# Kernel tuning notes

Hardware: AMD Instinct MI355X
Metric: run time of the kernel (lower is better)

Reference implementation:

```python
import jax, jax.numpy as jnp
import numpy as np

B, S, E, H = 4, 2048, 1024, 16
D = E // H  # head dim = 64


def setup_inputs() -> dict:
    key = jax.random.key(0)
    ks = jax.random.split(key, 9)
    sc = 1.0 / np.sqrt(E)
    x = jax.random.normal(ks[0], (B, S, E), dtype=jnp.float32)
    # causal mask: 1 = keep, 0 = masked -> -inf (matches masked_fill(mask==0, -inf))
    mask = jnp.broadcast_to(jnp.tril(jnp.ones((S, S), dtype=jnp.int32)), (B, S, S))
    return {
        "x": x,
        "mask": mask,
        "wq": jax.random.normal(ks[1], (E, E), dtype=jnp.float32) * sc,
        "bq": jax.random.normal(ks[2], (E,), dtype=jnp.float32) * sc,
        "wk": jax.random.normal(ks[3], (E, E), dtype=jnp.float32) * sc,
        "bk": jax.random.normal(ks[4], (E,), dtype=jnp.float32) * sc,
        "wv": jax.random.normal(ks[5], (E, E), dtype=jnp.float32) * sc,
        "bv": jax.random.normal(ks[6], (E,), dtype=jnp.float32) * sc,
        "wo": jax.random.normal(ks[7], (E, E), dtype=jnp.float32) * sc,
        "bo": jax.random.normal(ks[8], (E,), dtype=jnp.float32) * sc,
    }


def reference(x, mask, wq, bq, wk, bk, wv, bv, wo, bo):
    # nn.Linear: y = x @ W^T + b
    def proj(w, b):
        y = jnp.einsum('bse,fe->bsf', x, w) + b
        return y.reshape(B, S, H, D).transpose(0, 2, 1, 3)  # [B,H,S,D]

    q = proj(wq, bq)
    k = proj(wk, bk)
    v = proj(wv, bv)
    denom = jnp.asarray(np.sqrt(D), dtype=x.dtype)
    score = jnp.einsum('bhqd,bhkd->bhqk', q, k) / denom  # [B,H,S,S]
    score = jnp.where(mask[:, None, :, :] == 0, jnp.asarray(-jnp.inf, score.dtype), score)
    attn = jax.nn.softmax(score, axis=-1)
    out = jnp.einsum('bhqk,bhkd->bhqd', attn, v)  # [B,H,S,D]
    out = out.transpose(0, 2, 1, 3).reshape(B, S, E)
    return jnp.einsum('bse,fe->bsf', out, wo) + bo
```

## Files before the change

### kernel.cpp

```cpp
#include <hip/hip_runtime.h>
#include <cstdint>
#include <cstddef>

typedef unsigned short u16;
typedef __bf16 bf16;
typedef bf16 bf16x8 __attribute__((ext_vector_type(8)));
typedef bf16 bf16x4 __attribute__((ext_vector_type(4)));
typedef float f32x4 __attribute__((ext_vector_type(4)));
typedef u16 u16x8 __attribute__((ext_vector_type(8)));
typedef u16 u16x4 __attribute__((ext_vector_type(4)));

#define ASYNC16(g, l) __builtin_amdgcn_global_load_lds( \
    (const __attribute__((address_space(1))) void*)(g), \
    (__attribute__((address_space(3))) void*)(l), 16, 0, 0)

#define FENCE asm volatile("" ::: "memory")
#define BARRIER do { FENCE; __builtin_amdgcn_s_barrier(); FENCE; } while (0)
#define WAITVM(n) asm volatile("s_waitcnt vmcnt(" #n ")" ::: "memory")

__device__ __forceinline__ u16 f2bf(float f) {
  bf16 h = (bf16)f;
  return __builtin_bit_cast(u16, h);
}

__device__ __forceinline__ u16x4 pk4(float a, float b, float c, float d) {
  bf16x4 v = { (bf16)a, (bf16)b, (bf16)c, (bf16)d };
  return __builtin_bit_cast(u16x4, v);
}

__device__ __forceinline__ void store_out(u16* p, float v) { *p = f2bf(v); }
__device__ __forceinline__ void store_out(float* p, float v) { *p = v; }

__device__ __forceinline__ f32x4 mfma16(bf16x8 a, bf16x8 b, f32x4 c) {
  return __builtin_amdgcn_mfma_f32_16x16x32_bf16(a, b, c, 0, 0, 0);
}

__global__ void prep(const float* __restrict__ x,  const float* __restrict__ wq,
                     const float* __restrict__ wk, const float* __restrict__ wv,
                     const float* __restrict__ wo, const float* __restrict__ bq,
                     const float* __restrict__ bk,
                     u16* __restrict__ xb, u16* __restrict__ wqkb,
                     u16* __restrict__ wvb, u16* __restrict__ wob,
                     float* __restrict__ bqk, float scl)
{
  const int bid = blockIdx.x, tid = threadIdx.x;
  if (bid < 8192) {
    int i = bid * 256 + tid;
    float4 v = ((const float4*)x)[i];
    ((u16x4*)xb)[i] = pk4(v.x, v.y, v.z, v.w);
  } else if (bid < 12288) {
    int wsel = (bid - 8192) >> 10;
    int i = ((bid - 8192) & 1023) * 256 + tid;
    const float* src = wsel == 0 ? wq : wsel == 1 ? wk : wsel == 2 ? wv : wo;
    u16* dst = wsel == 0 ? wqkb : wsel == 1 ? wqkb + 1048576 : wsel == 2 ? wvb : wob;
    float s = wsel == 0 ? scl : 1.0f;
    float4 v = ((const float4*)src)[i];
    ((u16x4*)dst)[i] = pk4(v.x * s, v.y * s, v.z * s, v.w * s);
  } else {
    for (int i = tid; i < 1024; i += 256) {
      bqk[i] = bq[i] * scl;
      bqk[1024 + i] = bk[i];
    }
  }
}

template <typename OutT>
__device__ __forceinline__ void gemm256(
    u16* sA, u16* sB,
    const u16* __restrict__ A, const u16* __restrict__ Bm,
    const float* __restrict__ bias_col, const float* __restrict__ bias_row,
    OutT* __restrict__ C, int M, int N, int K, int bm, int bn)
{
  const int tid = threadIdx.x;
  const int w = tid >> 6, lane = tid & 63;
  const int quad = lane >> 4, l15 = lane & 15;
  const int wr = w >> 2, wc = w & 3;

  const int srow = tid >> 3;
  const int sslot = (tid & 7) ^ (srow & 7);
  const u16* gA = A + (size_t)(bm * 256 + srow) * K + sslot * 8;
  const u16* gB = Bm + (size_t)(bn * 256 + srow) * K + sslot * 8;
  u16* dA = sA + tid * 8;
  u16* dB = sB + tid * 8;
  const size_t rK64 = (size_t)64 * K, rK128 = (size_t)128 * K;

  auto stageA = [&](int c, int h, int kt) {
    const u16* s = gA + h * rK128 + kt * 64;
    u16* d = dA + c * 16384 + h * 8192;
    ASYNC16(s, d);
    ASYNC16(s + rK64, d + 4096);
  };
  auto stageB = [&](int c, int h, int kt) {
    const u16* s = gB + h * rK128 + kt * 64;
    u16* d = dB + c * 16384 + h * 8192;
    ASYNC16(s, d);
    ASYNC16(s + rK64, d + 4096);
  };

  f32x4 acc[8][4] = {};
  bf16x8 af[4][2];
  bf16x8 bf0[2][2];
  bf16x8 bf1[2][2];

  const int aRow = (wr * 128 + l15) * 64;
  const int bRow = (wc * 64 + l15) * 64;
  const int sw0 = (quad ^ (l15 & 7)) * 8;

#define LDA8(SRC, MH) do { \
    _Pragma("unroll") \
    for (int i = 0; i < 4; i++) { \
      af[i][0] = *(const bf16x8*)((SRC) + aRow + ((MH)*4 + i) * 1024 + sw0); \
      af[i][1] = *(const bf16x8*)((SRC) + aRow + ((MH)*4 + i) * 1024 + (sw0 ^ 32)); \
    } } while (0)

#define LDB4(DST, SRC, NH) do { \
    _Pragma("unroll") \
    for (int j = 0; j < 2; j++) { \
      DST[j][0] = *(const bf16x8*)((SRC) + bRow + ((NH)*2 + j) * 1024 + sw0); \
      DST[j][1] = *(const bf16x8*)((SRC) + bRow + ((NH)*2 + j) * 1024 + (sw0 ^ 32)); \
    } } while (0)

#define MMQ8(MH, NH, BF) do { \
    __builtin_amdgcn_s_setprio(1); \
    _Pragma("unroll") \
    for (int i = 0; i < 4; i++) { \
      acc[(MH)*4+i][(NH)*2+0] = mfma16(af[i][0], BF[0][0], acc[(MH)*4+i][(NH)*2+0]); \
      acc[(MH)*4+i][(NH)*2+0] = mfma16(af[i][1], BF[0][1], acc[(MH)*4+i][(NH)*2+0]); \
      acc[(MH)*4+i][(NH)*2+1] = mfma16(af[i][0], BF[1][0], acc[(MH)*4+i][(NH)*2+1]); \
      acc[(MH)*4+i][(NH)*2+1] = mfma16(af[i][1], BF[1][1], acc[(MH)*4+i][(NH)*2+1]); \
    } \
    __builtin_amdgcn_s_setprio(0); \
  } while (0)

  const int NT = K >> 6, NI = NT >> 1;

  stageB(0, 0, 0); stageB(0, 1, 0);
  stageA(0, 0, 0); stageA(0, 1, 0);
  stageB(1, 0, 1); stageB(1, 1, 1);
  WAITVM(4);
  BARRIER;

  u16* sA0 = sA;         u16* sA1 = sA + 16384;
  u16* sB0 = sB;         u16* sB1 = sB + 16384;

  for (int t = 0; t < NI; ++t) {
    const int k1 = 2 * t + 1, kn = 2 * t + 2, kn1 = 2 * t + 3;
    const bool more = (t + 1 < NI);

    LDA8(sA0, 0); LDB4(bf0, sB0, 0);
    stageA(1, 0, k1);
    BARRIER;
    MMQ8(0, 0, bf0);
    BARRIER;

    LDB4(bf1, sB0, 1);
    stageA(1, 1, k1);
    BARRIER;
    MMQ8(0, 1, bf1);
    BARRIER;

    LDA8(sA0, 1);
    if (more) stageB(0, 0, kn);
    BARRIER;
    MMQ8(1, 1, bf1);
    BARRIER;

    if (more) { stageB(0, 1, kn); WAITVM(4); }
    else      { WAITVM(0); }
    BARRIER;
    MMQ8(1, 0, bf0);
    BARRIER;

    LDA8(sA1, 0); LDB4(bf0, sB1, 0);
    if (more) stageA(0, 0, kn);
    BARRIER;
    MMQ8(0, 0, bf0);
    BARRIER;

    LDB4(bf1, sB1, 1);
    if (more) stageA(0, 1, kn);
    BARRIER;
    MMQ8(0, 1, bf1);
    BARRIER;

    LDA8(sA1, 1);
    if (more) stageB(1, 0, kn1);
    BARRIER;
    MMQ8(1, 1, bf1);
    BARRIER;

    if (more) { stageB(1, 1, kn1); WAITVM(4); }
    BARRIER;
    MMQ8(1, 0, bf0);
    BARRIER;
  }

#pragma unroll
  for (int nt = 0; nt < 4; nt++) {
    const int cc = bn * 256 + wc * 64 + nt * 16 + l15;
    const float bc = bias_col ? bias_col[cc] : 0.f;
#pragma unroll
    for (int mt = 0; mt < 8; mt++) {
      const int r0 = bm * 256 + wr * 128 + mt * 16 + quad * 4;
      f32x4 v = acc[mt][nt];
#pragma unroll
      for (int ri = 0; ri < 4; ri++) {
        const float bb = bc + (bias_row ? bias_row[r0 + ri] : 0.f);
        store_out(&C[(size_t)(r0 + ri) * N + cc], v[ri] + bb);
      }
    }
  }
#undef LDA8
#undef LDB4
#undef MMQ8
}

template <typename OutT>
__device__ __forceinline__ void gemm128(
    u16* sA, u16* sB,
    const u16* __restrict__ A, const u16* __restrict__ Bm,
    const float* __restrict__ bias_col, const float* __restrict__ bias_row,
    OutT* __restrict__ C, int M, int N, int K, int bm, int bn)
{
  const int tid = threadIdx.x;
  const int w = tid >> 6, lane = tid & 63;
  const int quad = lane >> 4, l15 = lane & 15;
  const int wr = w >> 2, wc = w & 3;

  const int srow = tid >> 3;
  const int sslot = (tid & 7) ^ (srow & 7);
  const u16* gA = A + (size_t)(bm * 128 + srow) * K + sslot * 8;
  const u16* gB = Bm + (size_t)(bn * 256 + srow) * K + sslot * 8;
  u16* dA = sA + tid * 8;
  u16* dB = sB + tid * 8;
  const size_t rK64 = (size_t)64 * K;

  auto stage0 = [&](int c, int kt) {
    const u16* a = gA + kt * 64;
    u16* da = dA + c * 8192;
    ASYNC16(a, da);
    ASYNC16(a + rK64, da + 4096);
    ASYNC16(gB + kt * 64, dB + c * 16384);
  };
  auto stage1 = [&](int c, int kt) {
    const u16* b = gB + kt * 64;
    u16* db = dB + c * 16384;
    ASYNC16(b + rK64,     db + 4096);
    ASYNC16(b + 2 * rK64, db + 8192);
    ASYNC16(b + 3 * rK64, db + 12288);
  };

  f32x4 acc[4][4] = {};
  bf16x8 af[4][2];
  bf16x8 bfr[2][2];

  const int aRow = (wr * 64 + l15) * 64;
  const int bRow = (wc * 64 + l15) * 64;
  const int sw0 = (quad ^ (l15 & 7)) * 8;

#define LDA(SRC) do { \
    _Pragma("unroll") \
    for (int i = 0; i < 4; i++) { \
      af[i][0] = *(const bf16x8*)((SRC) + aRow + i * 1024 + sw0); \
      af[i][1] = *(const bf16x8*)((SRC) + aRow + i * 1024 + (sw0 ^ 32)); \
    } } while (0)

#define LDB(SRC, NH) do { \
    _Pragma("unroll") \
    for (int j = 0; j < 2; j++) { \
      bfr[j][0] = *(const bf16x8*)((SRC) + bRow + ((NH)*2 + j) * 1024 + sw0); \
      bfr[j][1] = *(const bf16x8*)((SRC) + bRow + ((NH)*2 + j) * 1024 + (sw0 ^ 32)); \
    } } while (0)

#define MMQ(NH) do { \
    __builtin_amdgcn_s_setprio(1); \
    _Pragma("unroll") \
    for (int i = 0; i < 4; i++) { \
      acc[i][(NH)*2+0] = mfma16(af[i][0], bfr[0][0], acc[i][(NH)*2+0]); \
      acc[i][(NH)*2+0] = mfma16(af[i][1], bfr[0][1], acc[i][(NH)*2+0]); \
      acc[i][(NH)*2+1] = mfma16(af[i][0], bfr[1][0], acc[i][(NH)*2+1]); \
      acc[i][(NH)*2+1] = mfma16(af[i][1], bfr[1][1], acc[i][(NH)*2+1]); \
    } \
    __builtin_amdgcn_s_setprio(0); \
  } while (0)

  const int NT = K >> 6;

  stage0(0, 0); stage1(0, 0);
  stage0(1, 1); stage1(1, 1);
  WAITVM(6);
  BARRIER;

  for (int t = 0; t < NT; ++t) {
    const int c = t % 3, c2 = (t + 2) % 3;
    const bool more = (t + 2 < NT);
    const u16* SA = sA + c * 8192;
    const u16* SB = sB + c * 16384;

    LDA(SA); LDB(SB, 0);
    if (more) stage0(c2, t + 2);
    BARRIER;
    MMQ(0);
    BARRIER;

    LDB(SB, 1);
    if (more) {
      stage1(c2, t + 2);
      WAITVM(6);
    } else if (t == NT - 2) {
      WAITVM(0);
    }
    BARRIER;
    MMQ(1);
    BARRIER;
  }

#pragma unroll
  for (int nh = 0; nh < 2; nh++) {
#pragma unroll
    for (int j = 0; j < 2; j++) {
      const int cc = bn * 256 + wc * 64 + nh * 32 + j * 16 + l15;
      const float bc = bias_col ? bias_col[cc] : 0.f;
#pragma unroll
      for (int i = 0; i < 4; i++) {
        const int r0 = bm * 128 + wr * 64 + i * 16 + quad * 4;
        f32x4 v = acc[i][nh * 2 + j];
#pragma unroll
        for (int ri = 0; ri < 4; ri++) {
          const float bb = bc + (bias_row ? bias_row[r0 + ri] : 0.f);
          store_out(&C[(size_t)(r0 + ri) * N + cc], v[ri] + bb);
        }
      }
    }
  }
#undef LDA
#undef LDB
#undef MMQ
}

__global__ __launch_bounds__(512, 2) void gemm_qkv(
    const u16* __restrict__ xb, const u16* __restrict__ wqkb,
    const u16* __restrict__ wvb, const float* __restrict__ bqk,
    const float* __restrict__ bv, u16* __restrict__ qk, u16* __restrict__ vt)
{
  __shared__ __align__(16) u16 pool[73728];
  const int id = blockIdx.x;
  if (id < 256) {
    gemm256<u16>(pool, pool + 32768, xb, wqkb, bqk, nullptr, qk,
                 8192, 2048, 1024, id >> 3, id & 7);
  } else {
    const int j = id - 256;
    gemm128<u16>(pool, pool + 24576, wvb, xb, nullptr, bv, vt,
                 1024, 8192, 1024, j & 7, j >> 3);
  }
}

__global__ __launch_bounds__(512, 2) void gemm_out(
    const u16* __restrict__ ctx, const u16* __restrict__ wob,
    const float* __restrict__ bo, float* __restrict__ out)
{
  __shared__ __align__(16) u16 sA[3 * 8192];
  __shared__ __align__(16) u16 sB[3 * 16384];
  const int id = blockIdx.x;
  gemm128<float>(sA, sB, ctx, wob, bo, nullptr, out, 8192, 1024, 1024,
                 id >> 2, id & 3);
}

__global__ __launch_bounds__(256, 2) void fattn(
    const u16* __restrict__ QK, const u16* __restrict__ VT, u16* __restrict__ ctx)
{
  __shared__ u16 Kt[2][128 * 64];
  __shared__ u16 Vt[2][64 * 128];
  __shared__ u16 Pt[4 * 32 * 32];

  const int tid = threadIdx.x;
  const int w = tid >> 6, lane = tid & 63;
  const int quad = lane >> 4, l15 = lane & 15;
  const int p = blockIdx.x, h = blockIdx.y, b = blockIdx.z;
  const int nA = p + 1;
  const int sBs = 15 - p;

  const u16* QKb = QK + (size_t)b * 2048 * 2048;
  const u16* Kg = QKb + 1024 + h * 64 + ((tid & 7) ^ ((tid >> 3) & 7)) * 8;
  const u16* Vg = VT + (size_t)(h * 64) * 8192 + b * 2048 +
                  ((tid & 15) ^ ((tid >> 4) & 15)) * 8;

  u16* Pw = Pt + w * 1024;

  bf16x8 ones;
#pragma unroll
  for (int j = 0; j < 8; j++) ones[j] = (bf16)1.0f;

  bf16x8 qfA[2][2], qfB[2][2], qcur[2][2];
#pragma unroll
  for (int mt = 0; mt < 2; mt++)
#pragma unroll
    for (int ks = 0; ks < 2; ks++) {
      qfA[mt][ks] = *(const bf16x8*)(QKb +
          (size_t)(p  * 128 + w * 32 + mt * 16 + l15) * 2048 +
          h * 64 + ks * 32 + quad * 8);
      qfB[mt][ks] = *(const bf16x8*)(QKb +
          (size_t)(sBs * 128 + w * 32 + mt * 16 + l15) * 2048 +
          h * 64 + ks * 32 + quad * 8);
      qcur[mt][ks] = qfA[mt][ks];
    }

  auto stage = [&](int bi, int t) {
#pragma unroll
    for (int s = 0; s < 4; s++) {
      ASYNC16(Kg + (size_t)(t * 128 + s * 32 + (tid >> 3)) * 2048,
              Kt[bi] + (s * 256 + w * 64) * 8);
      ASYNC16(Vg + (size_t)(s * 16 + (tid >> 4)) * 8192 + t * 128,
              Vt[bi] + (s * 256 + w * 64) * 8);
    }
  };

  f32x4 oacc[4][2] = {};
  f32x4 lacc[2] = {};

  auto epi = [&](int sIdx) {
#pragma unroll
    for (int mt = 0; mt < 2; mt++) {
      float rl = 1.0f / lacc[mt][0];
      size_t row = (size_t)b * 2048 + sIdx * 128 + w * 32 + mt * 16 + l15;
#pragma unroll
      for (int dt = 0; dt < 4; dt++) {
        u16x4 o = pk4(oacc[dt][mt][0] * rl, oacc[dt][mt][1] * rl,
                      oacc[dt][mt][2] * rl, oacc[dt][mt][3] * rl);
        *(u16x4*)(ctx + row * 1024 + h * 64 + dt * 16 + quad * 4) = o;
      }
    }
  };

  int sCur = p, tcur = 0;
  stage(0, 0);

  for (int u = 0; u < 17; ++u) {
    const int cur = u & 1;
    if (u < 16) {
      const int tn = (u + 1 == nA) ? 0 : tcur + 1;
      stage(cur ^ 1, tn);
      WAITVM(8);
    } else {
      WAITVM(0);
    }
    BARRIER;

    const u16* Kc = Kt[cur];
    const u16* Vc = Vt[cur];

    f32x4 st[2][8] = {};
#pragma unroll
    for (int ks = 0; ks < 2; ks++) {
      bf16x8 kf[8];
#pragma unroll
      for (int nt = 0; nt < 8; nt++) {
        int row = nt * 16 + l15;
        kf[nt] = *(const bf16x8*)(Kc + (row * 8 + ((ks * 4 + quad) ^ (row & 7))) * 8);
      }
#pragma unroll
      for (int nt = 0; nt < 8; nt++) {
        st[0][nt] = mfma16(kf[nt], qcur[0][ks], st[0][nt]);
        st[1][nt] = mfma16(kf[nt], qcur[1][ks], st[1][nt]);
      }
    }

    if (tcur == sCur) {
#pragma unroll
      for (int mt = 0; mt < 2; mt++) {
        const int qg = w * 32 + mt * 16 + l15;
#pragma unroll
        for (int nt = 0; nt < 8; nt++)
#pragma unroll
          for (int r = 0; r < 4; r++)
            if (nt * 16 + quad * 4 + r > qg) st[mt][nt][r] = -3e38f;
      }
    }
#pragma unroll
    for (int mt = 0; mt < 2; mt++)
#pragma unroll
      for (int nt = 0; nt < 8; nt++)
#pragma unroll
        for (int r = 0; r < 4; r++)
          st[mt][nt][r] = exp2f(st[mt][nt][r]);

#pragma unroll
    for (int hf = 0; hf < 2; hf++) {
#pragma unroll
      for (int ks = 0; ks < 2; ks++) {
#pragma unroll
        for (int mt = 0; mt < 2; mt++) {
          const int row = mt * 16 + l15;
          const int swz = (row >> 1) & 3;
#pragma unroll
          for (int j = 0; j < 2; j++) {
            int nt = hf * 4 + ks * 2 + j;
            u16x4 pkv = pk4(st[mt][nt][0], st[mt][nt][1], st[mt][nt][2], st[mt][nt][3]);
            int c = (j * 2 + (quad >> 1)) ^ swz;
            *(u16x4*)(Pw + (row << 5) + (c << 3) + ((quad & 1) << 2)) = pkv;
          }
        }
        const int cq = quad ^ ((l15 >> 1) & 3);
        bf16x8 pf0 = *(const bf16x8*)(Pw + (l15 << 5) + (cq << 3));
        bf16x8 pf1 = *(const bf16x8*)(Pw + ((16 + l15) << 5) + (cq << 3));
        lacc[0] = mfma16(ones, pf0, lacc[0]);
        lacc[1] = mfma16(ones, pf1, lacc[1]);
#pragma unroll
        for (int dt = 0; dt < 4; dt++) {
          int vrow = dt * 16 + l15;
          bf16x8 vf = *(const bf16x8*)(Vc + (vrow * 16 + ((hf * 8 + ks * 4 + quad) ^ (vrow & 15))) * 8);
          oacc[dt][0] = mfma16(vf, pf0, oacc[dt][0]);
          oacc[dt][1] = mfma16(vf, pf1, oacc[dt][1]);
        }
      }
    }
    BARRIER;

    if (u == nA - 1) {
      epi(p);
#pragma unroll
      for (int dt = 0; dt < 4; dt++) {
        oacc[dt][0] = f32x4{0.f, 0.f, 0.f, 0.f};
        oacc[dt][1] = f32x4{0.f, 0.f, 0.f, 0.f};
      }
      lacc[0] = f32x4{0.f, 0.f, 0.f, 0.f};
      lacc[1] = f32x4{0.f, 0.f, 0.f, 0.f};
#pragma unroll
      for (int mt = 0; mt < 2; mt++)
#pragma unroll
        for (int ks = 0; ks < 2; ks++) qcur[mt][ks] = qfB[mt][ks];
      sCur = sBs; tcur = 0;
    } else {
      tcur++;
    }
  }

  epi(sBs);
}

extern "C" void kernel_launch(void* const* d_in, const int* in_sizes, int n_in,
                              void* d_out, int out_size, void* d_ws, size_t ws_size,
                              hipStream_t stream)
{
  const float* x  = (const float*)d_in[0];
  const float* wq = (const float*)d_in[2];
  const float* bq = (const float*)d_in[3];
  const float* wk = (const float*)d_in[4];
  const float* bk = (const float*)d_in[5];
  const float* wv = (const float*)d_in[6];
  const float* bv = (const float*)d_in[7];
  const float* wo = (const float*)d_in[8];
  const float* bo = (const float*)d_in[9];

  const float SCL = 0.125f * 1.44269504088896f;

  char* ws = (char*)d_ws;
  u16*   xb   = (u16*)(ws);
  u16*   ctx  = (u16*)(ws);
  u16*   wqkb = (u16*)(ws + 16777216);
  u16*   wvb  = (u16*)(ws + 20971520);
  u16*   wob  = (u16*)(ws + 23068672);
  float* bqk  = (float*)(ws + 25165824);
  u16*   qk   = (u16*)(ws + 25174016);
  u16*   vt   = (u16*)(ws + 58728448);
  float* out  = (float*)d_out;

  prep<<<12289, 256, 0, stream>>>(x, wq, wk, wv, wo, bq, bk,
                                  xb, wqkb, wvb, wob, bqk, SCL);

  gemm_qkv<<<512, 512, 0, stream>>>(xb, wqkb, wvb, bqk, bv, qk, vt);
  fattn<<<dim3(8, 16, 4), 256, 0, stream>>>(qk, vt, ctx);
  gemm_out<<<256, 512, 0, stream>>>(ctx, wob, bo, out);
}
```

Measured before the change: 313.4 us.

## Split attention blocks into 64-row query tiles with single-buffered K/V

The flash-attention kernel now runs 128-thread blocks (2 waves) that each handle a pair of 64-row query tiles (p and 31-p), so the causal work stays balanced across a grid twice as large. K/V staging drops from double-buffered to a single buffer, and the diagonal mask gains a row-parity offset. The launch grid is reordered so heads are the fastest-varying dimension. The intent is more resident blocks and less LDS per block, giving higher occupancy to hide latency. In exchange the loads are no longer overlapped with the MFMA work inside a block, and each K/V tile is now fetched once per 64 query rows instead of once per 128.

After: 306.9 us. 2.1% less time.

```diff
diff --git a/kernel.cpp b/kernel.cpp
--- a/kernel.cpp
+++ b/kernel.cpp
@@ -366,24 +366,23 @@
                  id >> 2, id & 3);
 }
 
-__global__ __launch_bounds__(256, 2) void fattn(
+__global__ __launch_bounds__(128, 2) void fattn(
     const u16* __restrict__ QK, const u16* __restrict__ VT, u16* __restrict__ ctx)
 {
-  __shared__ u16 Kt[2][128 * 64];
-  __shared__ u16 Vt[2][64 * 128];
-  __shared__ u16 Pt[4 * 32 * 32];
+  __shared__ u16 Kt[128 * 64];
+  __shared__ u16 Vt[64 * 128];
+  __shared__ u16 Pt[2 * 32 * 32];
 
   const int tid = threadIdx.x;
   const int w = tid >> 6, lane = tid & 63;
   const int quad = lane >> 4, l15 = lane & 15;
-  const int p = blockIdx.x, h = blockIdx.y, b = blockIdx.z;
-  const int nA = p + 1;
-  const int sBs = 15 - p;
+  const int h = blockIdx.x, p = blockIdx.y, b = blockIdx.z;
+  const int sB2 = 31 - p;
+  const int nA = (p >> 1) + 1;
 
   const u16* QKb = QK + (size_t)b * 2048 * 2048;
   const u16* Kg = QKb + 1024 + h * 64 + ((tid & 7) ^ ((tid >> 3) & 7)) * 8;
-  const u16* Vg = VT + (size_t)(h * 64) * 8192 + b * 2048 +
-                  ((tid & 15) ^ ((tid >> 4) & 15)) * 8;
+  const u16* Vg = VT + (size_t)(h * 64) * 8192 + b * 2048;
 
   u16* Pw = Pt + w * 1024;
 
@@ -397,21 +396,23 @@
 #pragma unroll
     for (int ks = 0; ks < 2; ks++) {
       qfA[mt][ks] = *(const bf16x8*)(QKb +
-          (size_t)(p  * 128 + w * 32 + mt * 16 + l15) * 2048 +
+          (size_t)(p   * 64 + w * 32 + mt * 16 + l15) * 2048 +
           h * 64 + ks * 32 + quad * 8);
       qfB[mt][ks] = *(const bf16x8*)(QKb +
-          (size_t)(sBs * 128 + w * 32 + mt * 16 + l15) * 2048 +
+          (size_t)(sB2 * 64 + w * 32 + mt * 16 + l15) * 2048 +
           h * 64 + ks * 32 + quad * 8);
       qcur[mt][ks] = qfA[mt][ks];
     }
 
-  auto stage = [&](int bi, int t) {
-#pragma unroll
-    for (int s = 0; s < 4; s++) {
-      ASYNC16(Kg + (size_t)(t * 128 + s * 32 + (tid >> 3)) * 2048,
-              Kt[bi] + (s * 256 + w * 64) * 8);
-      ASYNC16(Vg + (size_t)(s * 16 + (tid >> 4)) * 8192 + t * 128,
-              Vt[bi] + (s * 256 + w * 64) * 8);
+  auto stage = [&](int t) {
+#pragma unroll
+    for (int s = 0; s < 8; s++) {
+      ASYNC16(Kg + (size_t)(t * 128 + s * 16 + (tid >> 3)) * 2048,
+              Kt + (s * 128 + w * 64) * 8);
+      const int vrow = s * 8 + (tid >> 4);
+      const int vcol = (tid & 15) ^ (vrow & 15);
+      ASYNC16(Vg + (size_t)vrow * 8192 + t * 128 + vcol * 8,
+              Vt + (s * 128 + w * 64) * 8);
     }
   };
 
@@ -422,7 +423,7 @@
 #pragma unroll
     for (int mt = 0; mt < 2; mt++) {
       float rl = 1.0f / lacc[mt][0];
-      size_t row = (size_t)b * 2048 + sIdx * 128 + w * 32 + mt * 16 + l15;
+      size_t row = (size_t)b * 2048 + sIdx * 64 + w * 32 + mt * 16 + l15;
 #pragma unroll
       for (int dt = 0; dt < 4; dt++) {
         u16x4 o = pk4(oacc[dt][mt][0] * rl, oacc[dt][mt][1] * rl,
@@ -432,22 +433,12 @@
     }
   };
 
-  int sCur = p, tcur = 0;
-  stage(0, 0);
+  int sCur = p, nCur = nA, tcur = 0;
 
   for (int u = 0; u < 17; ++u) {
-    const int cur = u & 1;
-    if (u < 16) {
-      const int tn = (u + 1 == nA) ? 0 : tcur + 1;
-      stage(cur ^ 1, tn);
-      WAITVM(8);
-    } else {
-      WAITVM(0);
-    }
-    BARRIER;
-
-    const u16* Kc = Kt[cur];
-    const u16* Vc = Vt[cur];
+    stage(tcur);
+    WAITVM(0);
+    BARRIER;
 
     f32x4 st[2][8] = {};
 #pragma unroll
@@ -456,7 +447,7 @@
 #pragma unroll
       for (int nt = 0; nt < 8; nt++) {
         int row = nt * 16 + l15;
-        kf[nt] = *(const bf16x8*)(Kc + (row * 8 + ((ks * 4 + quad) ^ (row & 7))) * 8);
+        kf[nt] = *(const bf16x8*)(Kt + (row * 8 + ((ks * 4 + quad) ^ (row & 7))) * 8);
       }
 #pragma unroll
       for (int nt = 0; nt < 8; nt++) {
@@ -465,10 +456,11 @@
       }
     }
 
-    if (tcur == sCur) {
+    if (tcur == nCur - 1) {
+      const int par = (sCur & 1) << 6;
 #pragma unroll
       for (int mt = 0; mt < 2; mt++) {
-        const int qg = w * 32 + mt * 16 + l15;
+        const int qg = w * 32 + mt * 16 + l15 + par;
 #pragma unroll
         for (int nt = 0; nt < 8; nt++)
 #pragma unroll
@@ -508,7 +500,7 @@
 #pragma unroll
         for (int dt = 0; dt < 4; dt++) {
           int vrow = dt * 16 + l15;
-          bf16x8 vf = *(const bf16x8*)(Vc + (vrow * 16 + ((hf * 8 + ks * 4 + quad) ^ (vrow & 15))) * 8);
+          bf16x8 vf = *(const bf16x8*)(Vt + (vrow * 16 + ((hf * 8 + ks * 4 + quad) ^ (vrow & 15))) * 8);
           oacc[dt][0] = mfma16(vf, pf0, oacc[dt][0]);
           oacc[dt][1] = mfma16(vf, pf1, oacc[dt][1]);
         }
@@ -529,13 +521,13 @@
       for (int mt = 0; mt < 2; mt++)
 #pragma unroll
         for (int ks = 0; ks < 2; ks++) qcur[mt][ks] = qfB[mt][ks];
-      sCur = sBs; tcur = 0;
+      sCur = sB2; nCur = (sB2 >> 1) + 1; tcur = 0;
     } else {
       tcur++;
     }
   }
 
-  epi(sBs);
+  epi(sB2);
 }
 
 extern "C" void kernel_launch(void* const* d_in, const int* in_sizes, int n_in,
@@ -569,6 +561,6 @@
                                   xb, wqkb, wvb, wob, bqk, SCL);
 
   gemm_qkv<<<512, 512, 0, stream>>>(xb, wqkb, wvb, bqk, bv, qk, vt);
-  fattn<<<dim3(8, 16, 4), 256, 0, stream>>>(qk, vt, ctx);
+  fattn<<<dim3(16, 16, 4), 128, 0, stream>>>(qk, vt, ctx);
   gemm_out<<<256, 512, 0, stream>>>(ctx, wob, bo, out);
 }
```
